# Optimization experiments

Measured on AMD Instinct MI355X. Metric: run time of the kernel, lower is better.

## Reference

```python
import jax, jax.numpy as jnp
import numpy as np

DIM = 64
N_EMBED = 512
COMMITMENT_COST = 0.25


def setup_inputs() -> dict:
    key = jax.random.key(0)
    k1, k2 = jax.random.split(key)
    z = jax.random.normal(k1, (64, 32, 32, DIM), dtype=jnp.float32)
    # nn.Embedding weight initialized uniform(-1/n_embed, 1/n_embed)
    embed_w = jax.random.uniform(
        k2, (N_EMBED, DIM), dtype=jnp.float32,
        minval=-1.0 / N_EMBED, maxval=1.0 / N_EMBED)
    return {"z": z, "embed_w": embed_w}


def reference(z, embed_w):
    # z: [B, H, W, D] -> flatten to [N, D]
    z_flat = z.reshape(-1, z.shape[-1])
    # squared L2 distances via ||a||^2 + ||b||^2 - 2 a.b : [N, n_embed]
    distances = (
        jnp.sum(z_flat ** 2, axis=1, keepdims=True)
        + jnp.sum(embed_w ** 2, axis=1)
        - 2.0 * jnp.matmul(z_flat, embed_w.T)
    )
    min_encoding_indices = jnp.argmin(distances, axis=1)[:, None]  # [N, 1]
    z_q = embed_w[min_encoding_indices].reshape(z.shape)  # gather + reshape
    commitment_loss = COMMITMENT_COST * jnp.mean(
        (z - jax.lax.stop_gradient(z_q)) ** 2)
    return (z_q, min_encoding_indices, commitment_loss)
```

## Files before the change

### kernel.cpp

```cpp
#include <hip/hip_runtime.h>

#define NROWS 65536
#define DIM   64
#define NE    512

#define PREY_BYTES 131072
#define YN_FLT     34816
#define CTR_FLT    1048576

typedef __attribute__((ext_vector_type(8)))  short bf16x8;
typedef __attribute__((ext_vector_type(16))) float f32x16;

static __device__ __forceinline__ unsigned short bf16rne(float x) {
    unsigned int u = __float_as_uint(x);
    u += 0x7FFFu + ((u >> 16) & 1u);
    return (unsigned short)(u >> 16);
}
static __device__ __forceinline__ float bf16tof(unsigned short h) {
    return __uint_as_float(((unsigned int)h) << 16);
}

__global__ __launch_bounds__(256) void vq_prep(
    const float* __restrict__ ew, float* out)
{
    const int r = blockIdx.x * 256 + threadIdx.x;
    if (r == 0) ((unsigned int*)(out + CTR_FLT))[0] = 0u;
    float a[64];
    const float4* src = (const float4*)(ew + (size_t)r * DIM);
    #pragma unroll
    for (int q = 0; q < 16; ++q) {
        float4 v = src[q];
        a[q*4+0]=v.x; a[q*4+1]=v.y; a[q*4+2]=v.z; a[q*4+3]=v.w;
    }
    float rc[8];
    #pragma unroll
    for (int j = 0; j < 8; ++j) rc[j] = __fmul_rn(a[j], a[j]);
    #pragma unroll
    for (int i = 8; i < 64; i += 8)
        #pragma unroll
        for (int j = 0; j < 8; ++j)
            rc[j] = __fadd_rn(rc[j], __fmul_rn(a[i+j], a[i+j]));
    float Y = __fadd_rn(__fadd_rn(__fadd_rn(rc[0],rc[1]),__fadd_rn(rc[2],rc[3])),
                        __fadd_rn(__fadd_rn(rc[4],rc[5]),__fadd_rn(rc[6],rc[7])));
    out[YN_FLT + r] = Y;
    unsigned short ynh = bf16rne(Y);
    unsigned short ynl = bf16rne(Y - bf16tof(ynh));
    bf16x8 py = {};
    py[0] = (short)ynh; py[1] = (short)ynl;
    *(bf16x8*)((char*)out + PREY_BYTES + r*16) = py;
    const int sw = (r & 7) << 4;
    char* base = (char*)out + (size_t)r * 256;
    #pragma unroll
    for (int c = 0; c < 8; ++c) {
        bf16x8 h, l;
        #pragma unroll
        for (int j = 0; j < 8; ++j) {
            float x = -2.0f * a[c*8+j];
            unsigned short hb = bf16rne(x);
            h[j] = (short)hb;
            l[j] = (short)bf16rne(x - bf16tof(hb));
        }
        int off = (c*16) ^ sw;
        *(bf16x8*)(base + off) = h;
        *(bf16x8*)(base + off + 128) = l;
    }
}

__global__ __launch_bounds__(256) void vq_mfma(
    const float* __restrict__ z, float* out)
{
    __shared__ __align__(16) char lds[65536 + 8192];
    const float* pre = out;
    const int tid  = threadIdx.x;
    const int lane = tid & 63;
    const int w    = tid >> 6;
    const int hh   = lane >> 5;
    const int l31  = lane & 31;
    const int zrow = blockIdx.x * 128 + w * 32 + l31;

    bf16x8 zh[4], zl[4];
    float xacc = 0.f;
    {
        const float* zp = z + (size_t)zrow * DIM + hh * 8;
        #pragma unroll
        for (int kt = 0; kt < 4; ++kt) {
            float4 p0 = *(const float4*)(zp + kt*16);
            float4 p1 = *(const float4*)(zp + kt*16 + 4);
            float a[8] = {p0.x,p0.y,p0.z,p0.w,p1.x,p1.y,p1.z,p1.w};
            bf16x8 hv, lv;
            #pragma unroll
            for (int j = 0; j < 8; ++j) {
                unsigned short hb = bf16rne(a[j]);
                hv[j] = (short)hb;
                lv[j] = (short)bf16rne(a[j] - bf16tof(hb));
                xacc  = fmaf(a[j], a[j], xacc);
            }
            zh[kt] = hv; zl[kt] = lv;
        }
    }

    #pragma unroll
    for (int i = 0; i < 2; ++i)
        *(float4*)(lds + 65536 + (tid + 256*i)*16) =
            *(const float4*)((const char*)pre + PREY_BYTES + (tid + 256*i)*16);

    const bf16x8 zero8 = {};
    bf16x8 bones = {};
    if (hh == 0) { bones[0] = (short)0x3F80; bones[1] = (short)0x3F80; }

    float d1 = 3.4e38f, d2 = 3.4e38f;
    int   i1 = 0;

    for (int h = 0; h < 2; ++h) {
        __syncthreads();
        #pragma unroll
        for (int i = 0; i < 16; ++i)
            *(float4*)(lds + tid*16 + i*4096) =
                *(const float4*)((const char*)pre + h*65536 + tid*16 + i*4096);
        __syncthreads();

        for (int t = 0; t < 8; ++t) {
            const int   arow  = t*32 + l31;
            const char* abase = lds + arow*256;
            const int   sw    = (arow & 7) << 4;
            f32x16 acc;
            #pragma unroll
            for (int g = 0; g < 16; ++g) acc[g] = 0.f;
            #pragma unroll
            for (int kt = 0; kt < 4; ++kt) {
                const int kb = (kt*32 + hh*16) ^ sw;
                bf16x8 ah = *(const bf16x8*)(abase + kb);
                bf16x8 al = *(const bf16x8*)(abase + kb + 128);
                acc = __builtin_amdgcn_mfma_f32_32x32x16_bf16(ah, zh[kt], acc, 0,0,0);
                acc = __builtin_amdgcn_mfma_f32_32x32x16_bf16(ah, zl[kt], acc, 0,0,0);
                acc = __builtin_amdgcn_mfma_f32_32x32x16_bf16(al, zh[kt], acc, 0,0,0);
            }
            bf16x8 ay = *(const bf16x8*)(lds + 65536 + (h*256 + t*32 + l31)*16);
            if (hh) ay = zero8;
            acc = __builtin_amdgcn_mfma_f32_32x32x16_bf16(ay, bones, acc, 0,0,0);

            const int ebase = h*256 + t*32 + 4*hh;
            #pragma unroll
            for (int g = 0; g < 16; ++g) {
                float d = acc[g];
                int   e = ebase + (g & 3) + 8*(g >> 2);
                d2 = fminf(fmaxf(d, d1), d2);
                bool bt = d < d1;
                i1 = bt ? e : i1;
                d1 = fminf(d, d1);
            }
        }
    }

    float od1 = __shfl_xor(d1, 32, 64);
    int   oi1 = __shfl_xor(i1, 32, 64);
    float od2 = __shfl_xor(d2, 32, 64);
    bool  oth = (od1 < d1) || (od1 == d1 && oi1 < i1);
    int   wi  = oth ? oi1 : i1;
    float s1  = fminf(d1, od1);
    float s2  = fminf(fmaxf(d1, od1), fminf(d2, od2));
    float Xs  = xacc + __shfl_xor(xacc, 32, 64) + 1e-3f;
    float ue  = __uint_as_float(__float_as_uint(Xs) & 0x7F800000u) * 1.1920929e-7f;
    bool  flag = (s2 - s1) < (2.0f * ue + 2e-6f);

    if (hh == 0) {
        out[(size_t)NROWS * DIM + zrow] = (float)wi;
        if (flag) {
            unsigned int* ctr = (unsigned int*)(out + CTR_FLT);
            unsigned int pos = atomicAdd(ctr, 1u);
            ctr[1 + pos] = (unsigned int)zrow;
        }
    }
}

__global__ __launch_bounds__(256) void vq_rescan(
    const float* __restrict__ z, const float* __restrict__ ew, float* out)
{
    __shared__ float zs[64];
    __shared__ float rd[4];
    __shared__ int   ri[4];
    const int tid  = threadIdx.x;
    const int lane = tid & 63;
    const int w    = tid >> 6;
    const unsigned int* ctr = (const unsigned int*)(out + CTR_FLT);
    const unsigned int count = ctr[0];

    for (unsigned int it = blockIdx.x; it < count; it += gridDim.x) {
        const int row = (int)ctr[1 + it];
        __syncthreads();
        if (tid < 16)
            *(float4*)(zs + tid*4) = *(const float4*)(z + (size_t)row * DIM + tid*4);
        __syncthreads();

        float rc[8];
        #pragma unroll
        for (int j = 0; j < 8; ++j) rc[j] = __fmul_rn(zs[j], zs[j]);
        #pragma unroll
        for (int i = 8; i < 64; i += 8)
            #pragma unroll
            for (int j = 0; j < 8; ++j)
                rc[j] = __fadd_rn(rc[j], __fmul_rn(zs[i+j], zs[i+j]));
        float xn = __fadd_rn(__fadd_rn(__fadd_rn(rc[0],rc[1]),__fadd_rn(rc[2],rc[3])),
                             __fadd_rn(__fadd_rn(rc[4],rc[5]),__fadd_rn(rc[6],rc[7])));

        float bd = 3.4e38f; int bi = NE;
        #pragma unroll
        for (int half = 0; half < 2; ++half) {
            int e = tid + half * 256;
            const float* ep = ew + (size_t)e * DIM;
            double m0 = 0.0, m1 = 0.0, m2 = 0.0, m3 = 0.0;
            #pragma unroll
            for (int q = 0; q < 16; ++q) {
                float4 ev = *(const float4*)(ep + q*4);
                m0 = fma((double)zs[q*4+0], (double)ev.x, m0);
                m1 = fma((double)zs[q*4+1], (double)ev.y, m1);
                m2 = fma((double)zs[q*4+2], (double)ev.z, m2);
                m3 = fma((double)zs[q*4+3], (double)ev.w, m3);
            }
            double m = (m0 + m1) + (m2 + m3);
            float W = __fadd_rn(xn, out[YN_FLT + e]);
            float d = __fadd_rn(W, -(2.0f * (float)m));
            if (d < bd || (d == bd && e < bi)) { bd = d; bi = e; }
        }
        #pragma unroll
        for (int off = 32; off >= 1; off >>= 1) {
            float od = __shfl_xor(bd, off, 64);
            int   oi = __shfl_xor(bi, off, 64);
            if (od < bd || (od == bd && oi < bi)) { bd = od; bi = oi; }
        }
        if (lane == 0) { rd[w] = bd; ri[w] = bi; }
        __syncthreads();
        if (tid == 0) {
            float fd = rd[0]; int fi = ri[0];
            #pragma unroll
            for (int k = 1; k < 4; ++k)
                if (rd[k] < fd || (rd[k] == fd && ri[k] < fi)) { fd = rd[k]; fi = ri[k]; }
            out[(size_t)NROWS * DIM + row] = (float)fi;
        }
    }
}

__global__ __launch_bounds__(256) void vq_write_loss(
    const float* __restrict__ z, const float* __restrict__ ew,
    float* out, float* __restrict__ part)
{
    __shared__ int ridx[64];
    __shared__ float wsum[4];
    const int tid = threadIdx.x;
    const int R0  = blockIdx.x * 64;
    if (tid < 64)
        ridx[tid] = ((int)out[(size_t)NROWS * DIM + R0 + tid]) & (NE - 1);
    __syncthreads();
    float s = 0.f;
    #pragma unroll
    for (int i = 0; i < 4; ++i) {
        int f4  = tid + 256 * i;
        int row = f4 >> 4;
        int c4  = f4 & 15;
        float4 v  = *(const float4*)(ew + (size_t)ridx[row] * DIM + c4 * 4);
        float4 zz = *(const float4*)(z + (size_t)R0 * DIM + (size_t)f4 * 4);
        *(float4*)(out + (size_t)R0 * DIM + (size_t)f4 * 4) = v;
        float dx = zz.x - v.x, dy = zz.y - v.y, dz2 = zz.z - v.z, dw = zz.w - v.w;
        s = fmaf(dx, dx, s); s = fmaf(dy, dy, s);
        s = fmaf(dz2, dz2, s); s = fmaf(dw, dw, s);
    }
    #pragma unroll
    for (int off = 32; off >= 1; off >>= 1) s += __shfl_xor(s, off, 64);
    if ((tid & 63) == 0) wsum[tid >> 6] = s;
    __syncthreads();
    if (tid == 0) part[blockIdx.x] = wsum[0]+wsum[1]+wsum[2]+wsum[3];
}

__global__ __launch_bounds__(256) void vq_loss(
    const float* __restrict__ part, float* out)
{
    __shared__ double ws[4];
    int tid = threadIdx.x;
    double s = 0.0;
    #pragma unroll
    for (int i = 0; i < 4; ++i) s += (double)part[tid + 256*i];
    #pragma unroll
    for (int off = 32; off >= 1; off >>= 1) s += __shfl_xor(s, off, 64);
    if ((tid & 63) == 0) ws[tid >> 6] = s;
    __syncthreads();
    if (tid == 0)
        out[(size_t)NROWS*DIM + NROWS] =
            (float)(0.25 * (ws[0]+ws[1]+ws[2]+ws[3]) / (double)((size_t)NROWS*DIM));
}

extern "C" void kernel_launch(void* const* d_in, const int* in_sizes, int n_in,
                              void* d_out, int out_size, void* d_ws, size_t ws_size,
                              hipStream_t stream) {
    const float* z  = (const float*)d_in[0];
    const float* ew = (const float*)d_in[1];
    float* out  = (float*)d_out;
    float* part = (float*)d_ws;
    vq_prep      <<<2,    256, 0, stream>>>(ew, out);
    vq_mfma      <<<512,  256, 0, stream>>>(z, out);
    vq_rescan    <<<128,  256, 0, stream>>>(z, ew, out);
    vq_write_loss<<<1024, 256, 0, stream>>>(z, ew, out, part);
    vq_loss      <<<1,    256, 0, stream>>>(part, out);
}
```

Before: 45.47 us.

## Fuse rescan, gather-write and loss into the MFMA argmin kernel

Merges the MFMA distance/argmin kernel with the ambiguous-row rescan, the z_q gather-write and the loss reduction, so only two launches remain. Near-tie rows are now rescanned inside the owning block, tracked with LDS flag bits instead of a global atomic queue. The loss is taken from the minimum distance (||z||^2 plus the distance) rather than re-reading z, and is reduced through a fixed-point 64-bit atomic with a last-block ticket. This removes three launches and a second pass over z and the indices, but a block with many flagged rows now serializes the FP64 rescan, and the loss comes from the expanded-distance formula rather than a direct (z - z_q)^2 sum.

```diff
diff --git a/kernel.cpp b/kernel.cpp
--- a/kernel.cpp
+++ b/kernel.cpp
@@ -4,9 +4,11 @@
 #define DIM   64
 #define NE    512
 
-#define PREY_BYTES 131072
-#define YN_FLT     34816
-#define CTR_FLT    1048576
+#define WS_PRESPLIT 0
+#define WS_PREY     131072
+#define WS_YNORM    139264
+#define WS_ACC      141312
+#define WS_TICKET   141320
 
 typedef __attribute__((ext_vector_type(8)))  short bf16x8;
 typedef __attribute__((ext_vector_type(16))) float f32x16;
@@ -21,10 +23,13 @@
 }
 
 __global__ __launch_bounds__(256) void vq_prep(
-    const float* __restrict__ ew, float* out)
+    const float* __restrict__ ew, char* ws)
 {
     const int r = blockIdx.x * 256 + threadIdx.x;
-    if (r == 0) ((unsigned int*)(out + CTR_FLT))[0] = 0u;
+    if (r == 0) {
+        *(unsigned long long*)(ws + WS_ACC)    = 0ull;
+        *(unsigned long long*)(ws + WS_TICKET) = 0ull;
+    }
     float a[64];
     const float4* src = (const float4*)(ew + (size_t)r * DIM);
     #pragma unroll
@@ -42,14 +47,14 @@
             rc[j] = __fadd_rn(rc[j], __fmul_rn(a[i+j], a[i+j]));
     float Y = __fadd_rn(__fadd_rn(__fadd_rn(rc[0],rc[1]),__fadd_rn(rc[2],rc[3])),
                         __fadd_rn(__fadd_rn(rc[4],rc[5]),__fadd_rn(rc[6],rc[7])));
-    out[YN_FLT + r] = Y;
+    ((float*)(ws + WS_YNORM))[r] = Y;
     unsigned short ynh = bf16rne(Y);
     unsigned short ynl = bf16rne(Y - bf16tof(ynh));
     bf16x8 py = {};
     py[0] = (short)ynh; py[1] = (short)ynl;
-    *(bf16x8*)((char*)out + PREY_BYTES + r*16) = py;
+    *(bf16x8*)(ws + WS_PREY + r*16) = py;
     const int sw = (r & 7) << 4;
-    char* base = (char*)out + (size_t)r * 256;
+    char* base = ws + WS_PRESPLIT + (size_t)r * 256;
     #pragma unroll
     for (int c = 0; c < 8; ++c) {
         bf16x8 h, l;
@@ -66,17 +71,29 @@
     }
 }
 
-__global__ __launch_bounds__(256) void vq_mfma(
-    const float* __restrict__ z, float* out)
+__global__ __launch_bounds__(256) void vq_fused(
+    const float* __restrict__ z, const float* __restrict__ ew,
+    char* ws, float* out)
 {
-    __shared__ __align__(16) char lds[65536 + 8192];
-    const float* pre = out;
+    __shared__ __align__(16) char lds[65536];
+    __shared__ __align__(16) char ldsY[8192];
+    __shared__ int   rwin[128];
+    __shared__ float rdist[128];
+    __shared__ float rX[128];
+    __shared__ unsigned int flagbits[4];
+    __shared__ float rd4[4];
+    __shared__ int   ri4[4];
+    __shared__ float wred[4];
+
     const int tid  = threadIdx.x;
     const int lane = tid & 63;
     const int w    = tid >> 6;
     const int hh   = lane >> 5;
     const int l31  = lane & 31;
-    const int zrow = blockIdx.x * 128 + w * 32 + l31;
+    const int R0   = blockIdx.x * 128;
+    const int zrow = R0 + w * 32 + l31;
+
+    if (tid < 4) flagbits[tid] = 0;
 
     bf16x8 zh[4], zl[4];
     float xacc = 0.f;
@@ -101,8 +118,8 @@
 
     #pragma unroll
     for (int i = 0; i < 2; ++i)
-        *(float4*)(lds + 65536 + (tid + 256*i)*16) =
-            *(const float4*)((const char*)pre + PREY_BYTES + (tid + 256*i)*16);
+        *(float4*)(ldsY + (tid + 256*i)*16) =
+            *(const float4*)(ws + WS_PREY + (tid + 256*i)*16);
 
     const bf16x8 zero8 = {};
     bf16x8 bones = {};
@@ -116,7 +133,7 @@
         #pragma unroll
         for (int i = 0; i < 16; ++i)
             *(float4*)(lds + tid*16 + i*4096) =
-                *(const float4*)((const char*)pre + h*65536 + tid*16 + i*4096);
+                *(const float4*)(ws + WS_PRESPLIT + h*65536 + tid*16 + i*4096);
         __syncthreads();
 
         for (int t = 0; t < 8; ++t) {
@@ -135,7 +152,7 @@
                 acc = __builtin_amdgcn_mfma_f32_32x32x16_bf16(ah, zl[kt], acc, 0,0,0);
                 acc = __builtin_amdgcn_mfma_f32_32x32x16_bf16(al, zh[kt], acc, 0,0,0);
             }
-            bf16x8 ay = *(const bf16x8*)(lds + 65536 + (h*256 + t*32 + l31)*16);
+            bf16x8 ay = *(const bf16x8*)(ldsY + (h*256 + t*32 + l31)*16);
             if (hh) ay = zero8;
             acc = __builtin_amdgcn_mfma_f32_32x32x16_bf16(ay, bones, acc, 0,0,0);
 
@@ -159,133 +176,115 @@
     int   wi  = oth ? oi1 : i1;
     float s1  = fminf(d1, od1);
     float s2  = fminf(fmaxf(d1, od1), fminf(d2, od2));
-    float Xs  = xacc + __shfl_xor(xacc, 32, 64) + 1e-3f;
+    float Xf  = xacc + __shfl_xor(xacc, 32, 64);
+    float Xs  = Xf + 1e-3f;
     float ue  = __uint_as_float(__float_as_uint(Xs) & 0x7F800000u) * 1.1920929e-7f;
     bool  flag = (s2 - s1) < (2.0f * ue + 2e-6f);
 
     if (hh == 0) {
-        out[(size_t)NROWS * DIM + zrow] = (float)wi;
-        if (flag) {
-            unsigned int* ctr = (unsigned int*)(out + CTR_FLT);
-            unsigned int pos = atomicAdd(ctr, 1u);
-            ctr[1 + pos] = (unsigned int)zrow;
-        }
-    }
-}
-
-__global__ __launch_bounds__(256) void vq_rescan(
-    const float* __restrict__ z, const float* __restrict__ ew, float* out)
-{
-    __shared__ float zs[64];
-    __shared__ float rd[4];
-    __shared__ int   ri[4];
-    const int tid  = threadIdx.x;
-    const int lane = tid & 63;
-    const int w    = tid >> 6;
-    const unsigned int* ctr = (const unsigned int*)(out + CTR_FLT);
-    const unsigned int count = ctr[0];
-
-    for (unsigned int it = blockIdx.x; it < count; it += gridDim.x) {
-        const int row = (int)ctr[1 + it];
-        __syncthreads();
-        if (tid < 16)
-            *(float4*)(zs + tid*4) = *(const float4*)(z + (size_t)row * DIM + tid*4);
-        __syncthreads();
-
-        float rc[8];
-        #pragma unroll
-        for (int j = 0; j < 8; ++j) rc[j] = __fmul_rn(zs[j], zs[j]);
-        #pragma unroll
-        for (int i = 8; i < 64; i += 8)
-            #pragma unroll
-            for (int j = 0; j < 8; ++j)
-                rc[j] = __fadd_rn(rc[j], __fmul_rn(zs[i+j], zs[i+j]));
-        float xn = __fadd_rn(__fadd_rn(__fadd_rn(rc[0],rc[1]),__fadd_rn(rc[2],rc[3])),
-                             __fadd_rn(__fadd_rn(rc[4],rc[5]),__fadd_rn(rc[6],rc[7])));
-
-        float bd = 3.4e38f; int bi = NE;
-        #pragma unroll
-        for (int half = 0; half < 2; ++half) {
-            int e = tid + half * 256;
-            const float* ep = ew + (size_t)e * DIM;
-            double m0 = 0.0, m1 = 0.0, m2 = 0.0, m3 = 0.0;
+        int r = w*32 + l31;
+        rwin[r]  = wi;
+        rdist[r] = s1;
+        rX[r]    = Xf;
+        if (flag) atomicOr(&flagbits[r >> 5], 1u << (r & 31));
+    }
+    __syncthreads();
+
+    const float* yn = (const float*)(ws + WS_YNORM);
+    for (int wb = 0; wb < 4; ++wb) {
+        unsigned bits = flagbits[wb];
+        while (bits) {
+            int r = wb*32 + __ffs(bits) - 1;
+            bits &= bits - 1;
+            const float* zq = z + (size_t)(R0 + r) * DIM;
+            float zr[64];
             #pragma unroll
             for (int q = 0; q < 16; ++q) {
-                float4 ev = *(const float4*)(ep + q*4);
-                m0 = fma((double)zs[q*4+0], (double)ev.x, m0);
-                m1 = fma((double)zs[q*4+1], (double)ev.y, m1);
-                m2 = fma((double)zs[q*4+2], (double)ev.z, m2);
-                m3 = fma((double)zs[q*4+3], (double)ev.w, m3);
-            }
-            double m = (m0 + m1) + (m2 + m3);
-            float W = __fadd_rn(xn, out[YN_FLT + e]);
-            float d = __fadd_rn(W, -(2.0f * (float)m));
-            if (d < bd || (d == bd && e < bi)) { bd = d; bi = e; }
-        }
-        #pragma unroll
-        for (int off = 32; off >= 1; off >>= 1) {
-            float od = __shfl_xor(bd, off, 64);
-            int   oi = __shfl_xor(bi, off, 64);
-            if (od < bd || (od == bd && oi < bi)) { bd = od; bi = oi; }
-        }
-        if (lane == 0) { rd[w] = bd; ri[w] = bi; }
-        __syncthreads();
-        if (tid == 0) {
-            float fd = rd[0]; int fi = ri[0];
-            #pragma unroll
-            for (int k = 1; k < 4; ++k)
-                if (rd[k] < fd || (rd[k] == fd && ri[k] < fi)) { fd = rd[k]; fi = ri[k]; }
-            out[(size_t)NROWS * DIM + row] = (float)fi;
-        }
-    }
-}
-
-__global__ __launch_bounds__(256) void vq_write_loss(
-    const float* __restrict__ z, const float* __restrict__ ew,
-    float* out, float* __restrict__ part)
-{
-    __shared__ int ridx[64];
-    __shared__ float wsum[4];
-    const int tid = threadIdx.x;
-    const int R0  = blockIdx.x * 64;
-    if (tid < 64)
-        ridx[tid] = ((int)out[(size_t)NROWS * DIM + R0 + tid]) & (NE - 1);
-    __syncthreads();
-    float s = 0.f;
-    #pragma unroll
-    for (int i = 0; i < 4; ++i) {
+                float4 v = *(const float4*)(zq + q*4);
+                zr[q*4+0]=v.x; zr[q*4+1]=v.y; zr[q*4+2]=v.z; zr[q*4+3]=v.w;
+            }
+            float rc[8];
+            #pragma unroll
+            for (int j = 0; j < 8; ++j) rc[j] = __fmul_rn(zr[j], zr[j]);
+            #pragma unroll
+            for (int i = 8; i < 64; i += 8)
+                #pragma unroll
+                for (int j = 0; j < 8; ++j)
+                    rc[j] = __fadd_rn(rc[j], __fmul_rn(zr[i+j], zr[i+j]));
+            float xn = __fadd_rn(__fadd_rn(__fadd_rn(rc[0],rc[1]),__fadd_rn(rc[2],rc[3])),
+                                 __fadd_rn(__fadd_rn(rc[4],rc[5]),__fadd_rn(rc[6],rc[7])));
+            float bd = 3.4e38f; int bi = NE;
+            #pragma unroll
+            for (int half = 0; half < 2; ++half) {
+                int e = tid + half * 256;
+                const float* ep = ew + (size_t)e * DIM;
+                double m0 = 0.0, m1 = 0.0, m2 = 0.0, m3 = 0.0;
+                #pragma unroll
+                for (int q = 0; q < 16; ++q) {
+                    float4 ev = *(const float4*)(ep + q*4);
+                    m0 = fma((double)zr[q*4+0], (double)ev.x, m0);
+                    m1 = fma((double)zr[q*4+1], (double)ev.y, m1);
+                    m2 = fma((double)zr[q*4+2], (double)ev.z, m2);
+                    m3 = fma((double)zr[q*4+3], (double)ev.w, m3);
+                }
+                double m = (m0 + m1) + (m2 + m3);
+                float W = __fadd_rn(xn, yn[e]);
+                float d = __fadd_rn(W, -(2.0f * (float)m));
+                if (d < bd || (d == bd && e < bi)) { bd = d; bi = e; }
+            }
+            #pragma unroll
+            for (int off = 32; off >= 1; off >>= 1) {
+                float od = __shfl_xor(bd, off, 64);
+                int   oi = __shfl_xor(bi, off, 64);
+                if (od < bd || (od == bd && oi < bi)) { bd = od; bi = oi; }
+            }
+            if (lane == 0) { rd4[w] = bd; ri4[w] = bi; }
+            __syncthreads();
+            if (tid == 0) {
+                float fd = rd4[0]; int fi = ri4[0];
+                #pragma unroll
+                for (int k = 1; k < 4; ++k)
+                    if (rd4[k] < fd || (rd4[k] == fd && ri4[k] < fi)) { fd = rd4[k]; fi = ri4[k]; }
+                rwin[r]  = fi;
+                rdist[r] = fd;
+                rX[r]    = 0.f;
+            }
+            __syncthreads();
+        }
+    }
+
+    if (tid < 128)
+        out[(size_t)NROWS*DIM + R0 + tid] = (float)rwin[tid];
+
+    #pragma unroll
+    for (int i = 0; i < 8; ++i) {
         int f4  = tid + 256 * i;
         int row = f4 >> 4;
         int c4  = f4 & 15;
-        float4 v  = *(const float4*)(ew + (size_t)ridx[row] * DIM + c4 * 4);
-        float4 zz = *(const float4*)(z + (size_t)R0 * DIM + (size_t)f4 * 4);
+        float4 v = *(const float4*)(ew + (size_t)rwin[row] * DIM + c4 * 4);
         *(float4*)(out + (size_t)R0 * DIM + (size_t)f4 * 4) = v;
-        float dx = zz.x - v.x, dy = zz.y - v.y, dz2 = zz.z - v.z, dw = zz.w - v.w;
-        s = fmaf(dx, dx, s); s = fmaf(dy, dy, s);
-        s = fmaf(dz2, dz2, s); s = fmaf(dw, dw, s);
-    }
-    #pragma unroll
-    for (int off = 32; off >= 1; off >>= 1) s += __shfl_xor(s, off, 64);
-    if ((tid & 63) == 0) wsum[tid >> 6] = s;
+    }
+
+    float term = (tid < 128) ? (rX[tid] + rdist[tid]) : 0.f;
+    #pragma unroll
+    for (int off = 32; off >= 1; off >>= 1) term += __shfl_xor(term, off, 64);
+    if (lane == 0) wred[w] = term;
     __syncthreads();
-    if (tid == 0) part[blockIdx.x] = wsum[0]+wsum[1]+wsum[2]+wsum[3];
-}
-
-__global__ __launch_bounds__(256) void vq_loss(
-    const float* __restrict__ part, float* out)
-{
-    __shared__ double ws[4];
-    int tid = threadIdx.x;
-    double s = 0.0;
-    #pragma unroll
-    for (int i = 0; i < 4; ++i) s += (double)part[tid + 256*i];
-    #pragma unroll
-    for (int off = 32; off >= 1; off >>= 1) s += __shfl_xor(s, off, 64);
-    if ((tid & 63) == 0) ws[tid >> 6] = s;
-    __syncthreads();
-    if (tid == 0)
-        out[(size_t)NROWS*DIM + NROWS] =
-            (float)(0.25 * (ws[0]+ws[1]+ws[2]+ws[3]) / (double)((size_t)NROWS*DIM));
+    if (tid == 0) {
+        float part = wred[0] + wred[1] + wred[2] + wred[3];
+        unsigned long long q =
+            (unsigned long long)((double)part * 268435456.0 + 0.5);
+        atomicAdd((unsigned long long*)(ws + WS_ACC), q);
+        __threadfence();
+        unsigned int tk = atomicAdd((unsigned int*)(ws + WS_TICKET), 1u);
+        if (tk == 511u) {
+            unsigned long long tot =
+                atomicAdd((unsigned long long*)(ws + WS_ACC), 0ull);
+            out[(size_t)NROWS*DIM + NROWS] =
+                (float)(0.25 * ((double)tot / 268435456.0)
+                        / (double)((size_t)NROWS * DIM));
+        }
+    }
 }
 
 extern "C" void kernel_launch(void* const* d_in, const int* in_sizes, int n_in,
@@ -293,11 +292,8 @@
                               hipStream_t stream) {
     const float* z  = (const float*)d_in[0];
     const float* ew = (const float*)d_in[1];
-    float* out  = (float*)d_out;
-    float* part = (float*)d_ws;
-    vq_prep      <<<2,    256, 0, stream>>>(ew, out);
-    vq_mfma      <<<512,  256, 0, stream>>>(z, out);
-    vq_rescan    <<<128,  256, 0, stream>>>(z, ew, out);
-    vq_write_loss<<<1024, 256, 0, stream>>>(z, ew, out, part);
-    vq_loss      <<<1,    256, 0, stream>>>(part, out);
-}
+    float* out = (float*)d_out;
+    char*  ws  = (char*)d_ws;
+    vq_prep <<<2,   256, 0, stream>>>(ew, ws);
+    vq_fused<<<512, 256, 0, stream>>>(z, ew, ws, out);
+}
```

New measurement: 59.66 us. 31.2% more time.
